# Kernel optimization log

Hardware: AMD Instinct MI355X
Metric: run time of the kernel (lower is better)

Reference implementation:

```python
import jax, jax.numpy as jnp
import numpy as np

NUM_E = 100000
NUM_R = 500
HIDDEN = 64
BATCH = 32
GAMMA = 12.0
EPSILON = 2.0
EMB_RANGE = (GAMMA + EPSILON) / HIDDEN  # 0.21875
PI = 3.141592653589793


def setup_inputs() -> dict:
    key = jax.random.key(0)
    k1, k2, k3 = jax.random.split(key, 3)
    facts = jax.random.randint(k1, (BATCH, 3), 0, 1000, dtype=jnp.int64)  # col0<num_e, col1<2*num_r
    entity_embedding = jax.random.uniform(
        k2, (NUM_E, 2 * HIDDEN), dtype=jnp.float32, minval=-EMB_RANGE, maxval=EMB_RANGE)
    relation_embedding = jax.random.uniform(
        k3, (NUM_R * 2, HIDDEN), dtype=jnp.float32, minval=-EMB_RANGE, maxval=EMB_RANGE)
    return {"facts": facts, "entity_embedding": entity_embedding,
            "relation_embedding": relation_embedding}


def reference(facts, entity_embedding, relation_embedding):
    # Gather head/relation embeddings for the batch
    head = entity_embedding[facts[:, 0]]          # [B, 2D]
    relation = relation_embedding[facts[:, 1]]    # [B, D]

    re_head, im_head = jnp.split(head, 2, axis=1)           # [B, D] each
    re_tail, im_tail = jnp.split(entity_embedding, 2, axis=1)  # [E, D] each

    phase = relation / (EMB_RANGE / PI)
    re_rel = jnp.cos(phase)
    im_rel = jnp.sin(phase)

    # Complex rotation of head by relation: [B, D]
    re_rot = re_head * re_rel - im_head * im_rel
    im_rot = re_head * im_rel + im_head * re_rel

    # Broadcast difference against all entities: [B, E, D]
    re_diff = re_rot[:, None, :] - re_tail[None, :, :]
    im_diff = im_rot[:, None, :] - im_tail[None, :, :]

    # Per-component complex modulus, summed over dim -> [B, E]
    dist = jnp.sqrt(re_diff * re_diff + im_diff * im_diff).sum(axis=2)
    return GAMMA - dist
```

## Files before the change

### kernel.cpp

```cpp
#include <hip/hip_runtime.h>
#include <math.h>

#define NUM_E   100000
#define GAMMA_F 12.0f
#define EMB_RANGE_F 0.21875f
#define INV_TWO_EMB (1.0f / (2.0f * EMB_RANGE_F))

typedef float v4f __attribute__((ext_vector_type(4)));
typedef float v2f __attribute__((ext_vector_type(2)));

static __device__ __forceinline__ v2f pk_sub(v2f a, v2f b) {
    v2f d;
    asm("v_pk_add_f32 %0, %1, %2 neg_lo:[0,1] neg_hi:[0,1]"
        : "=v"(d) : "v"(a), "v"(b));
    return d;
}
static __device__ __forceinline__ v2f pk_mul(v2f a, v2f b) {
    v2f d;
    asm("v_pk_mul_f32 %0, %1, %2" : "=v"(d) : "v"(a), "v"(b));
    return d;
}
static __device__ __forceinline__ v2f pk_fma(v2f a, v2f b, v2f c) {
    v2f d;
    asm("v_pk_fma_f32 %0, %1, %2, %3" : "=v"(d) : "v"(a), "v"(b), "v"(c));
    return d;
}
static __device__ __forceinline__ float sq2(v2f dx, v2f dy) {
    v2f sq = pk_fma(dy, dy, pk_mul(dx, dx));
    return __builtin_amdgcn_sqrtf(sq.x) + __builtin_amdgcn_sqrtf(sq.y);
}
static __device__ __forceinline__ v2f lo2(v4f v) { return __builtin_shufflevector(v, v, 0, 1); }
static __device__ __forceinline__ v2f hi2(v4f v) { return __builtin_shufflevector(v, v, 2, 3); }

template <int CTRL>
static __device__ __forceinline__ float dpp_xor_add(float x) {
    int y = __builtin_amdgcn_update_dpp(0, __float_as_int(x), CTRL, 0xF, 0xF, true);
    return x + __int_as_float(y);
}

static __device__ __forceinline__ float dist_entity(
        v4f er0, v4f er1, v4f ei0, v4f ei1,
        const v2f RR[4], const v2f RI[4]) {
    v2f e2[4] = { lo2(er0), hi2(er0), lo2(er1), hi2(er1) };
    v2f i2[4] = { lo2(ei0), hi2(ei0), lo2(ei1), hi2(ei1) };
    float s0 = sq2(pk_sub(RR[0], e2[0]), pk_sub(RI[0], i2[0]));
    float s1 = sq2(pk_sub(RR[1], e2[1]), pk_sub(RI[1], i2[1]));
    float s2 = sq2(pk_sub(RR[2], e2[2]), pk_sub(RI[2], i2[2]));
    float s3 = sq2(pk_sub(RR[3], e2[3]), pk_sub(RI[3], i2[3]));
    float v = (s0 + s1) + (s2 + s3);
    v = dpp_xor_add<0xB1>(v);
    v = dpp_xor_add<0x4E>(v);
    v = dpp_xor_add<0x141>(v);
    return GAMMA_F - v;
}

#define LOADE(d0, d1, d2, d3, EIDX) do {                         \
    const float* _p = ent + (size_t)(EIDX) * 128 + dg * 8;       \
    d0 = *(const v4f*)(_p);      d1 = *(const v4f*)(_p + 4);     \
    d2 = *(const v4f*)(_p + 64); d3 = *(const v4f*)(_p + 68); } while (0)

__global__ __launch_bounds__(256, 2) void rotate_dist_fused(
        const int*   __restrict__ facts,
        const float* __restrict__ ent,
        const float* __restrict__ rel,
        float*       __restrict__ out) {
    const int t    = threadIdx.x;
    const int lane = t & 63;
    const int wv   = t >> 6;
    const int bq   = lane >> 3;
    const int dg   = lane & 7;
    const int b    = wv * 8 + bq;
    const int e0   = blockIdx.x * 16;

    v4f A0, A1, A2, A3, B0, B1, B2, B3;
    LOADE(A0, A1, A2, A3, e0);

    v2f RR[4], RI[4];
    {
        const int f0 = facts[b * 3 + 0];
        const int f1 = facts[b * 3 + 1];
        const float* hp = ent + (size_t)f0 * 128 + dg * 8;
        const float* rp = rel + (size_t)f1 * 64  + dg * 8;
        v4f hre0 = *(const v4f*)(hp);
        v4f hre1 = *(const v4f*)(hp + 4);
        v4f him0 = *(const v4f*)(hp + 64);
        v4f him1 = *(const v4f*)(hp + 68);
        v4f ph0  = *(const v4f*)(rp);
        v4f ph1  = *(const v4f*)(rp + 4);
        v4f rr0, rr1, ri0, ri1;
#pragma unroll
        for (int j = 0; j < 4; ++j) {
            float rev0 = ph0[j] * INV_TWO_EMB;
            float s0 = __builtin_amdgcn_sinf(rev0);
            float c0 = __builtin_amdgcn_cosf(rev0);
            rr0[j] = hre0[j] * c0 - him0[j] * s0;
            ri0[j] = hre0[j] * s0 + him0[j] * c0;
            float rev1 = ph1[j] * INV_TWO_EMB;
            float s1 = __builtin_amdgcn_sinf(rev1);
            float c1 = __builtin_amdgcn_cosf(rev1);
            rr1[j] = hre1[j] * c1 - him1[j] * s1;
            ri1[j] = hre1[j] * s1 + him1[j] * c1;
        }
        RR[0] = lo2(rr0); RR[1] = hi2(rr0); RR[2] = lo2(rr1); RR[3] = hi2(rr1);
        RI[0] = lo2(ri0); RI[1] = hi2(ri0); RI[2] = lo2(ri1); RI[3] = hi2(ri1);
    }

    float* obase = out + (size_t)b * NUM_E;
    const int elast = NUM_E - 1;

#pragma unroll 1
    for (int q = 0; q < 4; ++q) {
        const int eb = e0 + q * 4;
        v4f vout;
        LOADE(B0, B1, B2, B3, eb + 1);
        vout[0] = dist_entity(A0, A1, A2, A3, RR, RI);
        LOADE(A0, A1, A2, A3, eb + 2);
        vout[1] = dist_entity(B0, B1, B2, B3, RR, RI);
        LOADE(B0, B1, B2, B3, eb + 3);
        vout[2] = dist_entity(A0, A1, A2, A3, RR, RI);
        {
            int en = eb + 4; en = (en > elast) ? elast : en;
            LOADE(A0, A1, A2, A3, en);
        }
        vout[3] = dist_entity(B0, B1, B2, B3, RR, RI);
        if (dg == q) *(v4f*)(obase + eb) = vout;
    }
}

extern "C" void kernel_launch(void* const* d_in, const int* in_sizes, int n_in,
                              void* d_out, int out_size, void* d_ws, size_t ws_size,
                              hipStream_t stream) {
    const int*   facts = (const int*)d_in[0];
    const float* ent   = (const float*)d_in[1];
    const float* rel   = (const float*)d_in[2];
    float*       out   = (float*)d_out;
    (void)d_ws; (void)ws_size;

    rotate_dist_fused<<<dim3(NUM_E / 16), dim3(256), 0, stream>>>(facts, ent, rel, out);
}
```

Measured before the change: 137.3 us.

## Deepen entity-row prefetch to four in flight and overlap with head loads

```diff
diff --git a/kernel.cpp b/kernel.cpp
--- a/kernel.cpp
+++ b/kernel.cpp
@@ -72,21 +72,27 @@
     const int b    = wv * 8 + bq;
     const int e0   = blockIdx.x * 16;
 
-    v4f A0, A1, A2, A3, B0, B1, B2, B3;
-    LOADE(A0, A1, A2, A3, e0);
+    const int f0 = facts[b * 3 + 0];
+    const int f1 = facts[b * 3 + 1];
+    const float* hp = ent + (size_t)f0 * 128 + dg * 8;
+    const float* rp = rel + (size_t)f1 * 64  + dg * 8;
+    v4f hre0 = *(const v4f*)(hp);
+    v4f hre1 = *(const v4f*)(hp + 4);
+    v4f him0 = *(const v4f*)(hp + 64);
+    v4f him1 = *(const v4f*)(hp + 68);
+    v4f ph0  = *(const v4f*)(rp);
+    v4f ph1  = *(const v4f*)(rp + 4);
+
+    v4f P0a, P0b, P0c, P0d, P1a, P1b, P1c, P1d;
+    v4f P2a, P2b, P2c, P2d, P3a, P3b, P3c, P3d;
+    LOADE(P0a, P0b, P0c, P0d, e0 + 0);
+    LOADE(P1a, P1b, P1c, P1d, e0 + 1);
+    LOADE(P2a, P2b, P2c, P2d, e0 + 2);
+    LOADE(P3a, P3b, P3c, P3d, e0 + 3);
+    __builtin_amdgcn_sched_barrier(0);
 
     v2f RR[4], RI[4];
     {
-        const int f0 = facts[b * 3 + 0];
-        const int f1 = facts[b * 3 + 1];
-        const float* hp = ent + (size_t)f0 * 128 + dg * 8;
-        const float* rp = rel + (size_t)f1 * 64  + dg * 8;
-        v4f hre0 = *(const v4f*)(hp);
-        v4f hre1 = *(const v4f*)(hp + 4);
-        v4f him0 = *(const v4f*)(hp + 64);
-        v4f him1 = *(const v4f*)(hp + 68);
-        v4f ph0  = *(const v4f*)(rp);
-        v4f ph1  = *(const v4f*)(rp + 4);
         v4f rr0, rr1, ri0, ri1;
 #pragma unroll
         for (int j = 0; j < 4; ++j) {
@@ -108,23 +114,25 @@
     float* obase = out + (size_t)b * NUM_E;
     const int elast = NUM_E - 1;
 
-#pragma unroll 1
+#define SLOT(Pa, Pb, Pc, Pd, S) do {                               \
+        vout[S] = dist_entity(Pa, Pb, Pc, Pd, RR, RI);             \
+        int _en = eb + 4 + (S);                                    \
+        _en = (_en > elast) ? elast : _en;                         \
+        LOADE(Pa, Pb, Pc, Pd, _en);                                \
+        __builtin_amdgcn_sched_barrier(0);                         \
+    } while (0)
+
+#pragma unroll
     for (int q = 0; q < 4; ++q) {
         const int eb = e0 + q * 4;
         v4f vout;
-        LOADE(B0, B1, B2, B3, eb + 1);
-        vout[0] = dist_entity(A0, A1, A2, A3, RR, RI);
-        LOADE(A0, A1, A2, A3, eb + 2);
-        vout[1] = dist_entity(B0, B1, B2, B3, RR, RI);
-        LOADE(B0, B1, B2, B3, eb + 3);
-        vout[2] = dist_entity(A0, A1, A2, A3, RR, RI);
-        {
-            int en = eb + 4; en = (en > elast) ? elast : en;
-            LOADE(A0, A1, A2, A3, en);
-        }
-        vout[3] = dist_entity(B0, B1, B2, B3, RR, RI);
+        SLOT(P0a, P0b, P0c, P0d, 0);
+        SLOT(P1a, P1b, P1c, P1d, 1);
+        SLOT(P2a, P2b, P2c, P2d, 2);
+        SLOT(P3a, P3b, P3c, P3d, 3);
         if (dg == q) *(v4f*)(obase + eb) = vout;
     }
+#undef SLOT
 }
 
 extern "C" void kernel_launch(void* const* d_in, const int* in_sizes, int n_in,
```

Result: faster. 133.4 us (-2.8%).

## Stage entity tiles into LDS with async loads in a persistent double-buffered loop

Applied to the files above, without the earlier changes.

```diff
diff --git a/kernel.cpp b/kernel.cpp
--- a/kernel.cpp
+++ b/kernel.cpp
@@ -5,6 +5,10 @@
 #define GAMMA_F 12.0f
 #define EMB_RANGE_F 0.21875f
 #define INV_TWO_EMB (1.0f / (2.0f * EMB_RANGE_F))
+
+#define TILE_E  16
+#define NT      (NUM_E / TILE_E)
+#define GRID    2048
 
 typedef float v4f __attribute__((ext_vector_type(4)));
 typedef float v2f __attribute__((ext_vector_type(2)));
@@ -54,26 +58,35 @@
     return GAMMA_F - v;
 }
 
-#define LOADE(d0, d1, d2, d3, EIDX) do {                         \
-    const float* _p = ent + (size_t)(EIDX) * 128 + dg * 8;       \
-    d0 = *(const v4f*)(_p);      d1 = *(const v4f*)(_p + 4);     \
-    d2 = *(const v4f*)(_p + 64); d3 = *(const v4f*)(_p + 68); } while (0)
+static __device__ __forceinline__ void stage_chunk(const float* g, float* l) {
+    __builtin_amdgcn_global_load_lds(
+        (const __attribute__((address_space(1))) void*)g,
+        (__attribute__((address_space(3))) void*)l,
+        16, 0, 0);
+}
 
 __global__ __launch_bounds__(256, 2) void rotate_dist_fused(
         const int*   __restrict__ facts,
         const float* __restrict__ ent,
         const float* __restrict__ rel,
         float*       __restrict__ out) {
+    __shared__ __align__(16) float sbuf[2][TILE_E * 128];
+
     const int t    = threadIdx.x;
     const int lane = t & 63;
     const int wv   = t >> 6;
     const int bq   = lane >> 3;
     const int dg   = lane & 7;
     const int b    = wv * 8 + bq;
-    const int e0   = blockIdx.x * 16;
 
-    v4f A0, A1, A2, A3, B0, B1, B2, B3;
-    LOADE(A0, A1, A2, A3, e0);
+    int tile = blockIdx.x;
+
+    {
+        const float* g = ent + (size_t)tile * (TILE_E * 128) + wv * 512 + lane * 4;
+        float* l = &sbuf[0][wv * 512];
+        stage_chunk(g, l);
+        stage_chunk(g + 256, l + 256);
+    }
 
     v2f RR[4], RI[4];
     {
@@ -106,24 +119,40 @@
     }
 
     float* obase = out + (size_t)b * NUM_E;
-    const int elast = NUM_E - 1;
 
-#pragma unroll 1
-    for (int q = 0; q < 4; ++q) {
-        const int eb = e0 + q * 4;
-        v4f vout;
-        LOADE(B0, B1, B2, B3, eb + 1);
-        vout[0] = dist_entity(A0, A1, A2, A3, RR, RI);
-        LOADE(A0, A1, A2, A3, eb + 2);
-        vout[1] = dist_entity(B0, B1, B2, B3, RR, RI);
-        LOADE(B0, B1, B2, B3, eb + 3);
-        vout[2] = dist_entity(A0, A1, A2, A3, RR, RI);
-        {
-            int en = eb + 4; en = (en > elast) ? elast : en;
-            LOADE(A0, A1, A2, A3, en);
+    int cur = 0;
+    __syncthreads();
+
+    while (true) {
+        const int nxt = tile + GRID;
+        if (nxt < NT) {
+            const float* g = ent + (size_t)nxt * (TILE_E * 128) + wv * 512 + lane * 4;
+            float* l = &sbuf[cur ^ 1][wv * 512];
+            stage_chunk(g, l);
+            stage_chunk(g + 256, l + 256);
         }
-        vout[3] = dist_entity(B0, B1, B2, B3, RR, RI);
-        if (dg == q) *(v4f*)(obase + eb) = vout;
+
+        const float* csrc = &sbuf[cur][0];
+        float* op = obase + tile * TILE_E;
+#pragma unroll
+        for (int q = 0; q < 4; ++q) {
+            v4f vout;
+#pragma unroll
+            for (int i = 0; i < 4; ++i) {
+                const float* ep = csrc + (q * 4 + i) * 128 + dg * 8;
+                v4f er0 = *(const v4f*)(ep);
+                v4f er1 = *(const v4f*)(ep + 4);
+                v4f ei0 = *(const v4f*)(ep + 64);
+                v4f ei1 = *(const v4f*)(ep + 68);
+                vout[i] = dist_entity(er0, er1, ei0, ei1, RR, RI);
+            }
+            if (dg == q) *(v4f*)(op + q * 4) = vout;
+        }
+
+        if (nxt >= NT) break;
+        __syncthreads();
+        cur ^= 1;
+        tile = nxt;
     }
 }
 
@@ -136,5 +165,5 @@
     float*       out   = (float*)d_out;
     (void)d_ws; (void)ws_size;
 
-    rotate_dist_fused<<<dim3(NUM_E / 16), dim3(256), 0, stream>>>(facts, ent, rel, out);
+    rotate_dist_fused<<<dim3(GRID), dim3(256), 0, stream>>>(facts, ent, rel, out);
 }
```

Result: faster. 116.5 us (-15.2%).
